# Kernel tuning notes

Hardware: AMD Instinct MI355X
Metric: run time of the kernel (lower is better)

The kernel has to match this reference:

```python
import jax, jax.numpy as jnp
import numpy as np

# 4D conv dimension numbers: N=batch, C/I/O=channels, T,Z,Y,X = 4 spatial dims
DN = ('NCTZYX', 'OITZYX', 'NCTZYX')
PAD = [(1, 1)] * 4  # padding=1 on each of the 4 spatial dims


def setup_inputs() -> dict:
    key = jax.random.key(0)
    kx, kw = jax.random.split(key)
    B, Cin, Cout = 1, 16, 4
    T, D, H, Wd = 10, 32, 64, 64
    K = 3
    x = jax.random.normal(kx, (B, Cin, T, D, H, Wd), dtype=jnp.float32)
    # xavier_uniform over [Cout, Cin, 3,3,3,3]
    fan_in = Cin * K ** 4
    fan_out = Cout * K ** 4
    limit = float(np.sqrt(6.0 / (fan_in + fan_out)))
    W = jax.random.uniform(kw, (Cout, Cin, K, K, K, K), dtype=jnp.float32,
                           minval=-limit, maxval=limit)
    b = jnp.zeros((Cout,), dtype=jnp.float32)
    return {"x": x, "W": W, "b": b}


def reference(x, W, b):
    # True 4D convolution (stride 1, padding 1, 'same' output) + channel softmax
    y = jax.lax.conv_general_dilated(
        x, W,
        window_strides=(1, 1, 1, 1),
        padding=PAD,
        dimension_numbers=DN,
    )
    y = y + b[None, :, None, None, None, None]
    return jax.nn.softmax(y, axis=1)
```

## Files before the change

kernel.cpp:

```cpp
#include <hip/hip_runtime.h>
#include <hip/hip_bf16.h>

#define CIN  16
#define COUT 4
#define TT   10
#define ZZ   32
#define YY   64
#define XX   64

constexpr int SX_CI = TT * ZZ * YY * XX;
constexpr int SX_T  = ZZ * YY * XX;
constexpr int SX_Z  = YY * XX;
constexpr int WCO   = CIN * 81;

constexpr int XT_TB = ZZ * YY * XX * CIN * 2;
constexpr int XT_ZB = YY * XX * CIN * 2;
constexpr int XT_YB = XX * CIN * 2;
constexpr size_t XT_BYTES = (size_t)TT * XT_TB;
constexpr size_t BTAB     = XT_BYTES;
constexpr size_t ZOFF     = BTAB + 9 * 2048;
constexpr size_t WS_NEED  = ZOFF + 2048;

typedef short  short8 __attribute__((ext_vector_type(8)));
typedef float  f32x4  __attribute__((ext_vector_type(4)));

__device__ __forceinline__ unsigned short f2bf(float f) {
    union { __hip_bfloat16 h; unsigned short u; } c;
    c.h = __float2bfloat16(f);
    return c.u;
}
__device__ __forceinline__ unsigned int pk(float a, float b) {
    return (unsigned int)f2bf(a) | ((unsigned int)f2bf(b) << 16);
}
__device__ __forceinline__ int swz16(int c) { return (c ^ ((c >> 3) & 1)) * 16; }

__global__ __launch_bounds__(256) void transpose_x(const float* __restrict__ x,
                                                   char* __restrict__ ws) {
    const int lane = threadIdx.x & 63;
    const int w    = threadIdx.x >> 6;
    const int yq = blockIdx.x, z = blockIdx.y, t = blockIdx.z;
    const size_t ebase = (size_t)t * SX_T + (size_t)z * SX_Z;
#pragma unroll
    for (int pass = 0; pass < 2; ++pass) {
        const int ypair = yq * 16 + w * 4 + pass * 2;
        float2 v[16];
#pragma unroll
        for (int ci = 0; ci < 16; ++ci)
            v[ci] = *(const float2*)(x + (size_t)ci * SX_CI + ebase +
                                     (size_t)ypair * XX + lane * 2);
        const int yy = ypair + (lane >> 5);
        const int xb = 2 * (lane & 31);
        char* rowp = ws + (((size_t)t * ZZ + z) * YY + yy) * 2048;
#pragma unroll
        for (int e = 0; e < 2; ++e) {
            const int xp = xb + e;
#pragma unroll
            for (int hh = 0; hh < 2; ++hh) {
                uint4 d;
                d.x = pk(e ? v[8*hh+0].y : v[8*hh+0].x, e ? v[8*hh+1].y : v[8*hh+1].x);
                d.y = pk(e ? v[8*hh+2].y : v[8*hh+2].x, e ? v[8*hh+3].y : v[8*hh+3].x);
                d.z = pk(e ? v[8*hh+4].y : v[8*hh+4].x, e ? v[8*hh+5].y : v[8*hh+5].x);
                d.w = pk(e ? v[8*hh+6].y : v[8*hh+6].x, e ? v[8*hh+7].y : v[8*hh+7].x);
                *(uint4*)(rowp + swz16(2 * xp + hh)) = d;
            }
        }
    }
}

__global__ void prep_B(const float* __restrict__ W, char* __restrict__ ws) {
    const int g = blockIdx.x * 256 + threadIdx.x;
    if (g < 1152) {
        const int p = g >> 7, rem = g & 127, frag = rem >> 6, L = rem & 63;
        const int q = L >> 4, n = L & 15, co = n & 3, dx = n >> 2;
        const int dt = p / 3, dz = p % 3;
        unsigned int d[4];
#pragma unroll
        for (int j = 0; j < 4; ++j) {
            float v0 = 0.f, v1 = 0.f;
            if (dx < 3) {
                if (frag == 0) {
                    const int dy = q >> 1;
                    const int ci0 = (q & 1) * 8 + 2 * j;
                    v0 = W[(co * CIN + ci0) * 81 + dt * 27 + dz * 9 + dy * 3 + dx];
                    v1 = W[(co * CIN + ci0 + 1) * 81 + dt * 27 + dz * 9 + dy * 3 + dx];
                } else if (q < 2) {
                    const int ci0 = q * 8 + 2 * j;
                    v0 = W[(co * CIN + ci0) * 81 + dt * 27 + dz * 9 + 6 + dx];
                    v1 = W[(co * CIN + ci0 + 1) * 81 + dt * 27 + dz * 9 + 6 + dx];
                }
            }
            d[j] = pk(v0, v1);
        }
        *(uint4*)(ws + BTAB + (size_t)p * 2048 + frag * 1024 + (size_t)L * 16) =
            make_uint4(d[0], d[1], d[2], d[3]);
    } else if (g < 1280) {
        *(uint4*)(ws + ZOFF + (size_t)(g - 1152) * 16) = make_uint4(0, 0, 0, 0);
    }
}

#define GL16(SRC, DST) __builtin_amdgcn_global_load_lds( \
    (const __attribute__((address_space(1))) unsigned int*)(SRC), \
    (__attribute__((address_space(3))) unsigned int*)(DST), 16, 0, 0)

#define LROW 21
__global__ __launch_bounds__(256, 3) void conv_mfma(
        const char* __restrict__ ws,
        const float* __restrict__ bias,
        float* __restrict__ out) {
    __shared__ char smem[2 * 18 * 2048];
    const int lane = threadIdx.x;
    const int wid  = __builtin_amdgcn_readfirstlane(threadIdx.y);
    const int yq = blockIdx.x, z0 = blockIdx.y, t0 = blockIdx.z;
    const int y0 = yq * 16;
    const int m = lane & 15, q = lane >> 4, h = q & 1, dyA = q >> 1;
    const int e2 = 2 * m + h;
    const int wid4 = wid * 4;
    const bool qlo = q < 2;

    f32x4 acc[4][4];
#pragma unroll
    for (int r = 0; r < 4; ++r)
#pragma unroll
        for (int xt = 0; xt < 4; ++xt) acc[r][xt] = (f32x4){0.f, 0.f, 0.f, 0.f};

#define STAGE(P) { \
    const int dtS = (P) / 3, dzS = (P) % 3; \
    const int t_in = t0 + dtS - 1, z_in = z0 + dzS - 1; \
    const bool pv = ((unsigned)t_in < TT) && ((unsigned)z_in < ZZ); \
    const int pbase = pv ? (t_in * XT_TB + z_in * XT_ZB) : 0; \
    char* bbS = smem + ((P) & 1) * 36864; \
    _Pragma("unroll") \
    for (int k = 0; k < 9; ++k) { \
        const int rw = (wid + 4 * k) >> 1; \
        const int hf = ((wid + 4 * k) & 1) * 1024; \
        const int y_in = y0 - 1 + rw; \
        const bool rv = pv && ((unsigned)y_in < YY); \
        const char* srcS = ws + (rv ? (size_t)(pbase + y_in * XT_YB) : ZOFF) \
                              + hf + lane * 16; \
        GL16(srcS, bbS + rw * 2048 + hf + lane * 16); \
    } }

#define COMPUTE(P) { \
    const char* bbC = smem + ((P) & 1) * 36864; \
    const short8 BfA = *(const short8*)(ws + BTAB + (P) * 2048 + lane * 16); \
    const short8 BfB = *(const short8*)(ws + BTAB + (P) * 2048 + 1024 + lane * 16); \
    _Pragma("unroll") \
    for (int r = 0; r < 4; ++r) { \
        _Pragma("unroll") \
        for (int xt = 0; xt < 4; ++xt) { \
            const int sw = swz16(32 * xt + e2); \
            const short8 fa = *(const short8*)(bbC + (wid4 + r + dyA) * 2048 + sw); \
            short8 fb = *(const short8*)(bbC + (wid4 + r + 2) * 2048 + sw); \
            fb = qlo ? fb : (short8)0; \
            acc[r][xt] = __builtin_amdgcn_mfma_f32_16x16x32_bf16(fa, BfA, acc[r][xt], 0, 0, 0); \
            acc[r][xt] = __builtin_amdgcn_mfma_f32_16x16x32_bf16(fb, BfB, acc[r][xt], 0, 0, 0); \
        } } }

    STAGE(0)
    STAGE(1) __syncthreads(); COMPUTE(0) __syncthreads();
    STAGE(2) __syncthreads(); COMPUTE(1) __syncthreads();
    STAGE(3) __syncthreads(); COMPUTE(2) __syncthreads();
    STAGE(4) __syncthreads(); COMPUTE(3) __syncthreads();
    STAGE(5) __syncthreads(); COMPUTE(4) __syncthreads();
    STAGE(6) __syncthreads(); COMPUTE(5) __syncthreads();
    STAGE(7) __syncthreads(); COMPUTE(6) __syncthreads();
    STAGE(8) __syncthreads(); COMPUTE(7) __syncthreads();
    COMPUTE(8)
    __syncthreads();
#undef STAGE
#undef COMPUTE

    const float bi0 = bias[0], bi1 = bias[1], bi2 = bias[2], bi3 = bias[3];
    float* swave = (float*)smem + wid * (66 * LROW);
    if (lane < LROW) {
        swave[lane] = 0.f;
        swave[65 * LROW + lane] = 0.f;
    }
    const int colw = lane & 15;
    const int rowq = (lane >> 4) * 4 + 1;
#pragma unroll
    for (int r = 0; r < 4; ++r) {
#pragma unroll
        for (int xt = 0; xt < 4; ++xt)
#pragma unroll
            for (int reg = 0; reg < 4; ++reg)
                swave[(xt * 16 + rowq + reg) * LROW + colw] = acc[r][xt][reg];
        float lg0 = bi0, lg1 = bi1, lg2 = bi2, lg3 = bi3;
#pragma unroll
        for (int dx = 0; dx < 3; ++dx) {
            const float* sp = swave + (lane + dx) * LROW + dx * 4;
            lg0 += sp[0]; lg1 += sp[1]; lg2 += sp[2]; lg3 += sp[3];
        }
        const float mx = fmaxf(fmaxf(lg0, lg1), fmaxf(lg2, lg3));
        const float e0 = __expf(lg0 - mx);
        const float e1 = __expf(lg1 - mx);
        const float e2v = __expf(lg2 - mx);
        const float e3 = __expf(lg3 - mx);
        const float inv = 1.f / (e0 + e1 + e2v + e3);
        const int y = y0 + wid4 + r;
        float* op = out + (size_t)t0 * SX_T + (size_t)z0 * SX_Z + (size_t)y * XX + lane;
        op[0 * (size_t)SX_CI] = e0 * inv;
        op[1 * (size_t)SX_CI] = e1 * inv;
        op[2 * (size_t)SX_CI] = e2v * inv;
        op[3 * (size_t)SX_CI] = e3 * inv;
    }
}

__global__ __launch_bounds__(256, 4) void conv4d_softmax_vec(
        const float* __restrict__ x, const float* __restrict__ W,
        const float* __restrict__ b, float* __restrict__ out) {
    const int lane = threadIdx.x;
    const int xg = lane & 15, yl = lane >> 4;
    const int y = blockIdx.x * 16 + threadIdx.y * 4 + yl;
    const int z0 = blockIdx.y, t0 = blockIdx.z, x0 = xg * 4;
    float acc[COUT][4];
#pragma unroll
    for (int c = 0; c < COUT; ++c)
#pragma unroll
        for (int xi = 0; xi < 4; ++xi) acc[c][xi] = 0.f;
    for (int ci = 0; ci < CIN; ++ci) {
        const float* xc = x + (size_t)ci * SX_CI;
        const float* wc = W + ci * 81;
#pragma unroll
        for (int dt = 0; dt < 3; ++dt) {
            const int t_in = t0 + dt - 1;
            const int t_c = min(max(t_in, 0), TT - 1);
            const bool tv = (unsigned)t_in < TT;
#pragma unroll
            for (int dz = 0; dz < 3; ++dz) {
                const int z_in = z0 + dz - 1;
                const int z_c = min(max(z_in, 0), ZZ - 1);
                const bool tzvv = tv && ((unsigned)z_in < ZZ);
                const float* plane = xc + (size_t)t_c * SX_T + (size_t)z_c * SX_Z;
                const float* wb = wc + (dt * 3 + dz) * 9;
#pragma unroll
                for (int e = 0; e < 3; ++e) {
                    const int y_in = y + e - 1;
                    const int y_c = min(max(y_in, 0), YY - 1);
                    const bool v = tzvv && ((unsigned)y_in < YY);
                    float4 f = *(const float4*)(plane + y_c * XX + x0);
                    f.x = v ? f.x : 0.f; f.y = v ? f.y : 0.f;
                    f.z = v ? f.z : 0.f; f.w = v ? f.w : 0.f;
                    float hl = __shfl(f.w, (lane - 1) & 63, 64);
                    hl = (xg == 0) ? 0.f : hl;
                    float hr = __shfl(f.x, (lane + 1) & 63, 64);
                    hr = (xg == 15) ? 0.f : hr;
                    const float win[6] = {hl, f.x, f.y, f.z, f.w, hr};
#pragma unroll
                    for (int co = 0; co < COUT; ++co) {
                        const float* wp = wb + co * WCO + e * 3;
                        const float w0 = wp[0], w1 = wp[1], w2 = wp[2];
#pragma unroll
                        for (int xi = 0; xi < 4; ++xi) {
                            float a = acc[co][xi];
                            a = fmaf(win[xi], w0, a);
                            a = fmaf(win[xi + 1], w1, a);
                            a = fmaf(win[xi + 2], w2, a);
                            acc[co][xi] = a;
                        }
                    }
                }
            }
        }
    }
    const float b0 = b[0], b1 = b[1], b2 = b[2], b3 = b[3];
    float4 rr[COUT];
#pragma unroll
    for (int xi = 0; xi < 4; ++xi) {
        const float a0 = acc[0][xi] + b0, a1 = acc[1][xi] + b1;
        const float a2 = acc[2][xi] + b2, a3 = acc[3][xi] + b3;
        const float mm = fmaxf(fmaxf(a0, a1), fmaxf(a2, a3));
        const float e0 = __expf(a0 - mm), e1 = __expf(a1 - mm);
        const float e2 = __expf(a2 - mm), e3 = __expf(a3 - mm);
        const float inv = 1.f / (e0 + e1 + e2 + e3);
        ((float*)&rr[0])[xi] = e0 * inv; ((float*)&rr[1])[xi] = e1 * inv;
        ((float*)&rr[2])[xi] = e2 * inv; ((float*)&rr[3])[xi] = e3 * inv;
    }
    float* op = out + (size_t)t0 * SX_T + (size_t)z0 * SX_Z + (size_t)y * XX + x0;
#pragma unroll
    for (int co = 0; co < COUT; ++co)
        *(float4*)(op + (size_t)co * SX_CI) = rr[co];
}

extern "C" void kernel_launch(void* const* d_in, const int* in_sizes, int n_in,
                              void* d_out, int out_size, void* d_ws, size_t ws_size,
                              hipStream_t stream) {
    const float* x = (const float*)d_in[0];
    const float* W = (const float*)d_in[1];
    const float* b = (const float*)d_in[2];
    float* out = (float*)d_out;

    if (ws_size >= WS_NEED) {
        char* ws = (char*)d_ws;
        transpose_x<<<dim3(4, ZZ, TT), dim3(256), 0, stream>>>(x, ws);
        prep_B<<<dim3(5), dim3(256), 0, stream>>>(W, ws);
        conv_mfma<<<dim3(4, ZZ, TT), dim3(64, 4), 0, stream>>>(ws, b, out);
    } else {
        conv4d_softmax_vec<<<dim3(4, ZZ, TT), dim3(64, 4), 0, stream>>>(x, W, b, out);
    }
}
```

Measured before the change: 185.6 us.

## Single-buffer conv LDS for higher occupancy and rewrite transpose via LDS

The conv kernel drops its double-buffered LDS staging to a single buffer. That halves shared memory per block and raises the launch-bounds occupancy hint from 3 to 4 blocks, at the cost of no longer overlapping the next stage's global-to-LDS loads with the current compute. The input transpose now does coalesced float4 loads, packs channel pairs into a padded LDS tile, and writes contiguous 16-byte rows, replacing strided float2 gathers. The XOR swizzle and the explicit zero-masking of the second A fragment are removed; correctness then relies on the B fragment already being zero for those lanes.

```diff
diff --git a/kernel.cpp b/kernel.cpp
--- a/kernel.cpp
+++ b/kernel.cpp
@@ -32,37 +32,41 @@
 __device__ __forceinline__ unsigned int pk(float a, float b) {
     return (unsigned int)f2bf(a) | ((unsigned int)f2bf(b) << 16);
 }
-__device__ __forceinline__ int swz16(int c) { return (c ^ ((c >> 3) & 1)) * 16; }
-
+
+#define TXS 36
+#define TYS (64 * TXS)
 __global__ __launch_bounds__(256) void transpose_x(const float* __restrict__ x,
                                                    char* __restrict__ ws) {
+    __shared__ char lds[16 * TYS];
     const int lane = threadIdx.x & 63;
     const int w    = threadIdx.x >> 6;
     const int yq = blockIdx.x, z = blockIdx.y, t = blockIdx.z;
-    const size_t ebase = (size_t)t * SX_T + (size_t)z * SX_Z;
-#pragma unroll
-    for (int pass = 0; pass < 2; ++pass) {
-        const int ypair = yq * 16 + w * 4 + pass * 2;
-        float2 v[16];
-#pragma unroll
-        for (int ci = 0; ci < 16; ++ci)
-            v[ci] = *(const float2*)(x + (size_t)ci * SX_CI + ebase +
-                                     (size_t)ypair * XX + lane * 2);
-        const int yy = ypair + (lane >> 5);
-        const int xb = 2 * (lane & 31);
-        char* rowp = ws + (((size_t)t * ZZ + z) * YY + yy) * 2048;
-#pragma unroll
-        for (int e = 0; e < 2; ++e) {
-            const int xp = xb + e;
-#pragma unroll
-            for (int hh = 0; hh < 2; ++hh) {
-                uint4 d;
-                d.x = pk(e ? v[8*hh+0].y : v[8*hh+0].x, e ? v[8*hh+1].y : v[8*hh+1].x);
-                d.y = pk(e ? v[8*hh+2].y : v[8*hh+2].x, e ? v[8*hh+3].y : v[8*hh+3].x);
-                d.z = pk(e ? v[8*hh+4].y : v[8*hh+4].x, e ? v[8*hh+5].y : v[8*hh+5].x);
-                d.w = pk(e ? v[8*hh+6].y : v[8*hh+6].x, e ? v[8*hh+7].y : v[8*hh+7].x);
-                *(uint4*)(rowp + swz16(2 * xp + hh)) = d;
-            }
+    const int y0 = yq * 16;
+    const int rl = w * 4 + (lane >> 4);
+    const int x0 = (lane & 15) * 4;
+    const size_t gbase = (size_t)t * SX_T + (size_t)z * SX_Z +
+                         (size_t)(y0 + rl) * XX + x0;
+#pragma unroll
+    for (int cp = 0; cp < 8; ++cp) {
+        const float4 f0 = *(const float4*)(x + (size_t)(2 * cp + 0) * SX_CI + gbase);
+        const float4 f1 = *(const float4*)(x + (size_t)(2 * cp + 1) * SX_CI + gbase);
+        char* p = lds + rl * TYS + x0 * TXS + cp * 4;
+        *(unsigned int*)(p + 0 * TXS) = pk(f0.x, f1.x);
+        *(unsigned int*)(p + 1 * TXS) = pk(f0.y, f1.y);
+        *(unsigned int*)(p + 2 * TXS) = pk(f0.z, f1.z);
+        *(unsigned int*)(p + 3 * TXS) = pk(f0.w, f1.w);
+    }
+    __syncthreads();
+#pragma unroll
+    for (int s = 0; s < 4; ++s) {
+        const int r2 = w * 4 + s;
+        char* rowp = ws + (((size_t)t * ZZ + z) * YY + (y0 + r2)) * 2048;
+#pragma unroll
+        for (int half = 0; half < 2; ++half) {
+            const int c = half * 64 + lane;
+            const uint4 d = *(const uint4*)(lds + r2 * TYS + (c >> 1) * TXS +
+                                            (c & 1) * 16);
+            *(uint4*)(rowp + c * 16) = d;
         }
     }
 }
@@ -103,11 +107,11 @@
     (__attribute__((address_space(3))) unsigned int*)(DST), 16, 0, 0)
 
 #define LROW 21
-__global__ __launch_bounds__(256, 3) void conv_mfma(
+__global__ __launch_bounds__(256, 4) void conv_mfma(
         const char* __restrict__ ws,
         const float* __restrict__ bias,
         float* __restrict__ out) {
-    __shared__ char smem[2 * 18 * 2048];
+    __shared__ char smem[18 * 2048];
     const int lane = threadIdx.x;
     const int wid  = __builtin_amdgcn_readfirstlane(threadIdx.y);
     const int yq = blockIdx.x, z0 = blockIdx.y, t0 = blockIdx.z;
@@ -115,7 +119,6 @@
     const int m = lane & 15, q = lane >> 4, h = q & 1, dyA = q >> 1;
     const int e2 = 2 * m + h;
     const int wid4 = wid * 4;
-    const bool qlo = q < 2;
 
     f32x4 acc[4][4];
 #pragma unroll
@@ -128,7 +131,6 @@
     const int t_in = t0 + dtS - 1, z_in = z0 + dzS - 1; \
     const bool pv = ((unsigned)t_in < TT) && ((unsigned)z_in < ZZ); \
     const int pbase = pv ? (t_in * XT_TB + z_in * XT_ZB) : 0; \
-    char* bbS = smem + ((P) & 1) * 36864; \
     _Pragma("unroll") \
     for (int k = 0; k < 9; ++k) { \
         const int rw = (wid + 4 * k) >> 1; \
@@ -137,36 +139,32 @@
         const bool rv = pv && ((unsigned)y_in < YY); \
         const char* srcS = ws + (rv ? (size_t)(pbase + y_in * XT_YB) : ZOFF) \
                               + hf + lane * 16; \
-        GL16(srcS, bbS + rw * 2048 + hf + lane * 16); \
+        GL16(srcS, smem + rw * 2048 + hf + lane * 16); \
     } }
 
 #define COMPUTE(P) { \
-    const char* bbC = smem + ((P) & 1) * 36864; \
     const short8 BfA = *(const short8*)(ws + BTAB + (P) * 2048 + lane * 16); \
     const short8 BfB = *(const short8*)(ws + BTAB + (P) * 2048 + 1024 + lane * 16); \
     _Pragma("unroll") \
     for (int r = 0; r < 4; ++r) { \
         _Pragma("unroll") \
         for (int xt = 0; xt < 4; ++xt) { \
-            const int sw = swz16(32 * xt + e2); \
-            const short8 fa = *(const short8*)(bbC + (wid4 + r + dyA) * 2048 + sw); \
-            short8 fb = *(const short8*)(bbC + (wid4 + r + 2) * 2048 + sw); \
-            fb = qlo ? fb : (short8)0; \
+            const int sw = (32 * xt + e2) * 16; \
+            const short8 fa = *(const short8*)(smem + (wid4 + r + dyA) * 2048 + sw); \
+            const short8 fb = *(const short8*)(smem + (wid4 + r + 2) * 2048 + sw); \
             acc[r][xt] = __builtin_amdgcn_mfma_f32_16x16x32_bf16(fa, BfA, acc[r][xt], 0, 0, 0); \
             acc[r][xt] = __builtin_amdgcn_mfma_f32_16x16x32_bf16(fb, BfB, acc[r][xt], 0, 0, 0); \
         } } }
 
-    STAGE(0)
-    STAGE(1) __syncthreads(); COMPUTE(0) __syncthreads();
-    STAGE(2) __syncthreads(); COMPUTE(1) __syncthreads();
-    STAGE(3) __syncthreads(); COMPUTE(2) __syncthreads();
-    STAGE(4) __syncthreads(); COMPUTE(3) __syncthreads();
-    STAGE(5) __syncthreads(); COMPUTE(4) __syncthreads();
-    STAGE(6) __syncthreads(); COMPUTE(5) __syncthreads();
-    STAGE(7) __syncthreads(); COMPUTE(6) __syncthreads();
-    STAGE(8) __syncthreads(); COMPUTE(7) __syncthreads();
-    COMPUTE(8)
-    __syncthreads();
+    STAGE(0) __syncthreads(); COMPUTE(0) __syncthreads();
+    STAGE(1) __syncthreads(); COMPUTE(1) __syncthreads();
+    STAGE(2) __syncthreads(); COMPUTE(2) __syncthreads();
+    STAGE(3) __syncthreads(); COMPUTE(3) __syncthreads();
+    STAGE(4) __syncthreads(); COMPUTE(4) __syncthreads();
+    STAGE(5) __syncthreads(); COMPUTE(5) __syncthreads();
+    STAGE(6) __syncthreads(); COMPUTE(6) __syncthreads();
+    STAGE(7) __syncthreads(); COMPUTE(7) __syncthreads();
+    STAGE(8) __syncthreads(); COMPUTE(8) __syncthreads();
 #undef STAGE
 #undef COMPUTE
 
```

New measurement: 184.7 us. Within noise of the previous version (-0.5%).
